# Kernel tuning notes

Measured on AMD Instinct MI355X. Metric: run time of the kernel, lower is better.

Reference implementation:

```python
import jax, jax.numpy as jnp
import numpy as np
from jax import lax


def setup_inputs() -> dict:
    key = jax.random.key(0)
    ks = jax.random.split(key, 5)
    B, Cin, H, W = 16, 64, 64, 64
    HID, K = 128, 3
    x = jax.random.normal(ks[0], (B, Cin, H, W), jnp.float32)
    w_is = jax.random.normal(ks[1], (4 * HID, Cin, 1, K), jnp.float32) * 0.05
    b_is = jax.random.normal(ks[2], (4 * HID,), jnp.float32) * 0.05
    w_ss = jax.random.normal(ks[3], (4 * HID, HID, 1, K), jnp.float32) * 0.05
    b_ss = jax.random.normal(ks[4], (4 * HID,), jnp.float32) * 0.05
    return {"x": x, "w_is": w_is, "b_is": b_is, "w_ss": w_ss, "b_ss": b_ss}


def reference(x, w_is, b_is, w_ss, b_ss):
    # Shapes: x [B,Cin,H,W]; w_is [4h,Cin,1,k]; w_ss [4h,h,1,k]
    hid = w_ss.shape[1]
    k = w_is.shape[-1]
    pad = k // 2

    # MaskedConv2d mask type 'B' on a (1,k) kernel: keep center and left taps,
    # zero everything strictly right of center.
    mask = (jnp.arange(k) <= pad).astype(x.dtype)  # [k]
    w_is_m = w_is * mask[None, None, None, :]

    # Input-to-state conv over the whole image at once: [B,4h,H,W]
    z_is = lax.conv_general_dilated(
        x, w_is_m, window_strides=(1, 1), padding=[(0, 0), (pad, pad)]
    ) + b_is[None, :, None, None]

    # State-to-state conv is a 1D conv along W: kernel [4h, h, k]
    w1 = w_ss[:, :, 0, :]

    def step(carry, z_row):
        h, c = carry  # each [B, hid, W]
        z = z_row + lax.conv_general_dilated(
            h, w1, window_strides=(1,), padding=[(pad, pad)],
            dimension_numbers=("NCH", "OIH", "NCH"),
        ) + b_ss[None, :, None]
        i_g = jax.nn.sigmoid(z[:, :hid])
        f_g = jax.nn.sigmoid(z[:, hid:2 * hid])
        o_g = jax.nn.sigmoid(z[:, 2 * hid:3 * hid])
        g = jnp.tanh(z[:, 3 * hid:])
        c = f_g * c + i_g * g
        h = o_g * jnp.tanh(c)
        return (h, c), h

    B, _, H, W = x.shape
    h0 = jnp.zeros((B, hid, W), x.dtype)
    c0 = jnp.zeros((B, hid, W), x.dtype)
    zs = jnp.transpose(z_is, (2, 0, 1, 3))  # [H, B, 4h, W]
    _, hs = lax.scan(step, (h0, c0), zs)    # hs: [H, B, hid, W]
    return jnp.transpose(hs, (1, 2, 0, 3))  # [B, hid, H, W]
```

## Files before the change

kernel.cpp:

```cpp
#include <hip/hip_runtime.h>
#include <hip/hip_bf16.h>

#define B_    16
#define CIN   64
#define Hn    64
#define Wn    64
#define HID   128
#define SXS2  72
#define SHS   136
#define NJC   8
#define NBLK  (B_ * NJC)

typedef __attribute__((ext_vector_type(8))) short bfrag_t;
typedef __attribute__((ext_vector_type(4))) float f4_t;

#define HBUF_SHORTS (B_ * Wn * HID)
#define HBUF_BYTES  (HBUF_SHORTS * 2)
#define FLG_STRIDE  256

static __device__ __forceinline__ short f2bf(float f) {
    union { __hip_bfloat16 h; short s; } u;
    u.h = __float2bfloat16(f);
    return u.s;
}
static __device__ __forceinline__ float sigm(float z)  { return 1.f / (1.f + __expf(-z)); }
static __device__ __forceinline__ float tanhf_(float z){ return 2.f / (1.f + __expf(-2.f * z)) - 1.f; }

#define BAR_LGKM() do { \
    asm volatile("s_waitcnt lgkmcnt(0)" ::: "memory"); \
    __builtin_amdgcn_s_barrier(); \
    __builtin_amdgcn_sched_barrier(0); \
} while (0)

extern "C" __global__ __launch_bounds__(256, 1)
void rowlstm_kernel(const float* __restrict__ x,
                    const float* __restrict__ w_is,
                    const float* __restrict__ b_is,
                    const float* __restrict__ w_ss,
                    const float* __restrict__ b_ss,
                    float* __restrict__ out,
                    unsigned char* __restrict__ ws)
{
    const int tid  = threadIdx.x;
    const int bid  = blockIdx.x;
    const int b    = bid & 15;
    const int jc   = bid >> 4;
    const int lane = tid & 63;
    const int wv   = tid >> 6;
    const int l15  = lane & 15;
    const int quad = lane >> 4;

    short*    hbuf0 = (short*)ws;
    unsigned* flags = (unsigned*)(ws + 2 * HBUF_BYTES + b * FLG_STRIDE);

    __shared__ alignas(16) short sH[66 * SHS];
    __shared__ alignas(16) short sX2[65 * SXS2];

    bfrag_t a_frag[4][16];
    #pragma unroll
    for (int mt = 0; mt < 4; ++mt) {
        const int co = mt * HID + jc * 16 + l15;
        #pragma unroll
        for (int kt = 0; kt < 16; ++kt) {
            const int kk0 = kt * 32 + quad * 8;
            const float* p;
            if      (kt < 2)  p = &w_is[(co * CIN + kk0)         * 3 + 0];
            else if (kt < 4)  p = &w_is[(co * CIN + (kk0 - 64))  * 3 + 1];
            else if (kt < 8)  p = &w_ss[(co * HID + (kk0 - 128)) * 3 + 0];
            else if (kt < 12) p = &w_ss[(co * HID + (kk0 - 256)) * 3 + 1];
            else              p = &w_ss[(co * HID + (kk0 - 384)) * 3 + 2];
            bfrag_t v;
            #pragma unroll
            for (int j = 0; j < 8; ++j) v[j] = f2bf(p[j * 3]);
            a_frag[mt][kt] = v;
        }
    }

    float bias[4][4];
    #pragma unroll
    for (int g = 0; g < 4; ++g) {
        #pragma unroll
        for (int r = 0; r < 4; ++r) {
            const int co = g * HID + jc * 16 + quad * 4 + r;
            bias[g][r] = b_is[co] + b_ss[co];
        }
    }

    {
        bfrag_t z8 = {0,0,0,0,0,0,0,0};
        if (tid < 8)  *(bfrag_t*)&sX2[tid * 8] = z8;
        if (tid < 16) {
            *(bfrag_t*)&sH[tid * 8] = z8;
            *(bfrag_t*)&sH[65 * SHS + tid * 8] = z8;
        }
    }

    float creg[4] = {0.f, 0.f, 0.f, 0.f};
    const int wp  = wv * 16 + l15;

    const int xw  = tid & 63;
    const int xc2 = tid >> 6;
    float xr[16];
    #pragma unroll
    for (int e = 0; e < 16; ++e)
        xr[e] = x[((b * CIN + xc2 * 16 + e) * Hn + 0) * Wn + xw];

    {
        bfrag_t v0, v1;
        #pragma unroll
        for (int e = 0; e < 8; ++e) { v0[e] = f2bf(xr[e]); v1[e] = f2bf(xr[e + 8]); }
        *(bfrag_t*)&sX2[(xw + 1) * SXS2 + xc2 * 16]     = v0;
        *(bfrag_t*)&sX2[(xw + 1) * SXS2 + xc2 * 16 + 8] = v1;
        #pragma unroll
        for (int e = 0; e < 16; ++e)
            xr[e] = x[((b * CIN + xc2 * 16 + e) * Hn + 1) * Wn + xw];
    }

    const int cig = tid & 15;
    const int w0  = tid >> 4;

    __syncthreads();

    for (int h = 0; h < Hn; ++h) {
        const short* rd_hb = hbuf0 + ((h & 1) ^ 1) * HBUF_SHORTS + b * Wn * HID;
        short*       wr_hb = hbuf0 + (h & 1) * HBUF_SHORTS + b * Wn * HID;

        union { bfrag_t f; unsigned long long q[2]; } hu0, hu1, hu2, hu3;
        if (h > 0) {
            const unsigned tgt = (unsigned)h;
            for (;;) {
                unsigned f = __hip_atomic_load(&flags[lane & 31],
                                               __ATOMIC_RELAXED, __HIP_MEMORY_SCOPE_AGENT);
                if (__all((int)(f >= tgt))) break;
                __builtin_amdgcn_s_sleep(1);
            }
            asm volatile("" ::: "memory");

            const unsigned long long* s0 = (const unsigned long long*)(rd_hb + (w0     ) * HID + cig * 8);
            const unsigned long long* s1 = (const unsigned long long*)(rd_hb + (w0 + 16) * HID + cig * 8);
            const unsigned long long* s2 = (const unsigned long long*)(rd_hb + (w0 + 32) * HID + cig * 8);
            const unsigned long long* s3 = (const unsigned long long*)(rd_hb + (w0 + 48) * HID + cig * 8);
            hu0.q[0] = __hip_atomic_load(s0,     __ATOMIC_RELAXED, __HIP_MEMORY_SCOPE_AGENT);
            hu0.q[1] = __hip_atomic_load(s0 + 1, __ATOMIC_RELAXED, __HIP_MEMORY_SCOPE_AGENT);
            hu1.q[0] = __hip_atomic_load(s1,     __ATOMIC_RELAXED, __HIP_MEMORY_SCOPE_AGENT);
            hu1.q[1] = __hip_atomic_load(s1 + 1, __ATOMIC_RELAXED, __HIP_MEMORY_SCOPE_AGENT);
            hu2.q[0] = __hip_atomic_load(s2,     __ATOMIC_RELAXED, __HIP_MEMORY_SCOPE_AGENT);
            hu2.q[1] = __hip_atomic_load(s2 + 1, __ATOMIC_RELAXED, __HIP_MEMORY_SCOPE_AGENT);
            hu3.q[0] = __hip_atomic_load(s3,     __ATOMIC_RELAXED, __HIP_MEMORY_SCOPE_AGENT);
            hu3.q[1] = __hip_atomic_load(s3 + 1, __ATOMIC_RELAXED, __HIP_MEMORY_SCOPE_AGENT);
        } else {
            hu0.q[0] = hu0.q[1] = 0ull; hu1.q[0] = hu1.q[1] = 0ull;
            hu2.q[0] = hu2.q[1] = 0ull; hu3.q[0] = hu3.q[1] = 0ull;
        }

        f4_t acc0 = {0.f,0.f,0.f,0.f}, acc1 = {0.f,0.f,0.f,0.f};
        f4_t acc2 = {0.f,0.f,0.f,0.f}, acc3 = {0.f,0.f,0.f,0.f};
        #pragma unroll
        for (int kt = 0; kt < 4; ++kt) {
            const short* src = &sX2[(wp + (kt >> 1)) * SXS2 + (kt & 1) * 32 + quad * 8];
            bfrag_t bf = *(const bfrag_t*)src;
            acc0 = __builtin_amdgcn_mfma_f32_16x16x32_bf16(a_frag[0][kt], bf, acc0, 0, 0, 0);
            acc1 = __builtin_amdgcn_mfma_f32_16x16x32_bf16(a_frag[1][kt], bf, acc1, 0, 0, 0);
            acc2 = __builtin_amdgcn_mfma_f32_16x16x32_bf16(a_frag[2][kt], bf, acc2, 0, 0, 0);
            acc3 = __builtin_amdgcn_mfma_f32_16x16x32_bf16(a_frag[3][kt], bf, acc3, 0, 0, 0);
        }

        *(bfrag_t*)&sH[(w0 +  1) * SHS + cig * 8] = hu0.f;
        *(bfrag_t*)&sH[(w0 + 17) * SHS + cig * 8] = hu1.f;
        *(bfrag_t*)&sH[(w0 + 33) * SHS + cig * 8] = hu2.f;
        *(bfrag_t*)&sH[(w0 + 49) * SHS + cig * 8] = hu3.f;
        BAR_LGKM();

        #pragma unroll
        for (int kt = 4; kt < 16; ++kt) {
            const short* src = &sH[(wp + ((kt - 4) >> 2)) * SHS + ((kt - 4) & 3) * 32 + quad * 8];
            bfrag_t bf = *(const bfrag_t*)src;
            acc0 = __builtin_amdgcn_mfma_f32_16x16x32_bf16(a_frag[0][kt], bf, acc0, 0, 0, 0);
            acc1 = __builtin_amdgcn_mfma_f32_16x16x32_bf16(a_frag[1][kt], bf, acc1, 0, 0, 0);
            acc2 = __builtin_amdgcn_mfma_f32_16x16x32_bf16(a_frag[2][kt], bf, acc2, 0, 0, 0);
            acc3 = __builtin_amdgcn_mfma_f32_16x16x32_bf16(a_frag[3][kt], bf, acc3, 0, 0, 0);
        }

        float hv[4];
        #pragma unroll
        for (int r = 0; r < 4; ++r) {
            float ig = sigm (acc0[r] + bias[0][r]);
            float fg = sigm (acc1[r] + bias[1][r]);
            float og = sigm (acc2[r] + bias[2][r]);
            float gg = tanhf_(acc3[r] + bias[3][r]);
            float c  = fg * creg[r] + ig * gg;
            creg[r]  = c;
            hv[r]    = og * tanhf_(c);
        }

        if (h + 1 < Hn) {
            unsigned p0 = (unsigned)(unsigned short)f2bf(hv[0]) |
                          ((unsigned)(unsigned short)f2bf(hv[1]) << 16);
            unsigned p1 = (unsigned)(unsigned short)f2bf(hv[2]) |
                          ((unsigned)(unsigned short)f2bf(hv[3]) << 16);
            unsigned long long pk = (unsigned long long)p0 | ((unsigned long long)p1 << 32);
            __hip_atomic_store((unsigned long long*)(wr_hb + wp * HID + jc * 16 + quad * 4),
                               pk, __ATOMIC_RELAXED, __HIP_MEMORY_SCOPE_AGENT);
            asm volatile("s_waitcnt vmcnt(0)" ::: "memory");
            if (lane == 0)
                __hip_atomic_store(&flags[jc * 4 + wv], (unsigned)(h + 1),
                                   __ATOMIC_RELAXED, __HIP_MEMORY_SCOPE_AGENT);
        }

        __syncthreads();

        if (h + 1 < Hn) {
            bfrag_t v0, v1;
            #pragma unroll
            for (int e = 0; e < 8; ++e) { v0[e] = f2bf(xr[e]); v1[e] = f2bf(xr[e + 8]); }
            *(bfrag_t*)&sX2[(xw + 1) * SXS2 + xc2 * 16]     = v0;
            *(bfrag_t*)&sX2[(xw + 1) * SXS2 + xc2 * 16 + 8] = v1;
        }

        #pragma unroll
        for (int r = 0; r < 4; ++r)
            out[((b * HID + jc * 16 + quad * 4 + r) * Hn + h) * Wn + wp] = hv[r];

        if (h + 2 < Hn) {
            #pragma unroll
            for (int e = 0; e < 16; ++e)
                xr[e] = x[((b * CIN + xc2 * 16 + e) * Hn + (h + 2)) * Wn + xw];
        }

        if (h + 1 < Hn)
            BAR_LGKM();
    }
}

extern "C" void kernel_launch(void* const* d_in, const int* in_sizes, int n_in,
                              void* d_out, int out_size, void* d_ws, size_t ws_size,
                              hipStream_t stream) {
    const float* x    = (const float*)d_in[0];
    const float* w_is = (const float*)d_in[1];
    const float* b_is = (const float*)d_in[2];
    const float* w_ss = (const float*)d_in[3];
    const float* b_ss = (const float*)d_in[4];
    float* out = (float*)d_out;
    unsigned char* ws = (unsigned char*)d_ws;

    hipMemsetAsync(ws + 2 * HBUF_BYTES, 0, B_ * FLG_STRIDE, stream);

    rowlstm_kernel<<<dim3(NBLK), dim3(256), 0, stream>>>(x, w_is, b_is, w_ss, b_ss, out, ws);
}
```

Baseline: 314.2 us.

## Co-locate each batch's blocks on one XCD and exchange state via local L2

Launches 256 blocks and has each one read its XCD id from a hardware register, then claim a role so that the 8 blocks sharing a batch element land on the same XCD when possible. Excess blocks exit. When a batch's group is all on one XCD, hidden state and flags go through an extra buffer using plain stores and sc0 loads that stay in the local L2 rather than agent-scope coherent accesses. This aims to cut the latency of the per-row inter-block handoff. It keeps a coherent fallback path with a poll timeout and dual-writes every row, which adds store traffic. It also relies on unverified assumptions about L2 coherence and the hwreg layout.

```diff
diff --git a/kernel.cpp b/kernel.cpp
--- a/kernel.cpp
+++ b/kernel.cpp
@@ -9,14 +9,18 @@
 #define SXS2  72
 #define SHS   136
 #define NJC   8
-#define NBLK  (B_ * NJC)
+#define NGRID 256
+#define POLL_TO 256
 
 typedef __attribute__((ext_vector_type(8))) short bfrag_t;
 typedef __attribute__((ext_vector_type(4))) float f4_t;
 
 #define HBUF_SHORTS (B_ * Wn * HID)
 #define HBUF_BYTES  (HBUF_SHORTS * 2)
-#define FLG_STRIDE  256
+#define DATA_A_OFF  0
+#define DATA_B_OFF  (2 * HBUF_BYTES)
+#define FLG_OFF     (4 * HBUF_BYTES)
+#define CLAIM_OFF   (FLG_OFF + B_ * 256)
 
 static __device__ __forceinline__ short f2bf(float f) {
     union { __hip_bfloat16 h; short s; } u;
@@ -42,16 +46,58 @@
                     unsigned char* __restrict__ ws)
 {
     const int tid  = threadIdx.x;
-    const int bid  = blockIdx.x;
-    const int b    = bid & 15;
-    const int jc   = bid >> 4;
     const int lane = tid & 63;
     const int wv   = tid >> 6;
     const int l15  = lane & 15;
     const int quad = lane >> 4;
 
-    short*    hbuf0 = (short*)ws;
-    unsigned* flags = (unsigned*)(ws + 2 * HBUF_BYTES + b * FLG_STRIDE);
+    __shared__ int sB, sJ, sM;
+    if (tid == 0) {
+        unsigned* cl = (unsigned*)(ws + CLAIM_OFF);
+        unsigned xcd;
+        asm volatile("s_getreg_b32 %0, hwreg(20, 0, 32)" : "=s"(xcd));
+        xcd &= 7u;
+        unsigned slot = __hip_atomic_fetch_add(&cl[xcd], 1u, __ATOMIC_RELAXED, __HIP_MEMORY_SCOPE_AGENT);
+        int role = (slot < 16u) ? (int)(xcd * 16u + slot) : -1;
+        __hip_atomic_fetch_add(&cl[8], 1u, __ATOMIC_RELEASE, __HIP_MEMORY_SCOPE_AGENT);
+        if (role < 0) {
+            while (__hip_atomic_load(&cl[8], __ATOMIC_ACQUIRE, __HIP_MEMORY_SCOPE_AGENT) < (unsigned)NGRID)
+                __builtin_amdgcn_s_sleep(8);
+            unsigned ovr = __hip_atomic_fetch_add(&cl[9], 1u, __ATOMIC_RELAXED, __HIP_MEMORY_SCOPE_AGENT);
+            unsigned base = 0;
+            for (int k = 0; k < 8 && role < 0; ++k) {
+                unsigned c = __hip_atomic_load(&cl[k], __ATOMIC_RELAXED, __HIP_MEMORY_SCOPE_AGENT);
+                if (c > 16u) c = 16u;
+                unsigned miss = 16u - c;
+                if (ovr < base + miss) role = (int)(k * 16u + c + (ovr - base));
+                base += miss;
+            }
+        }
+        int bb = -1, jj = 0, mm = 0;
+        if (role >= 0) {
+            bb = (role >> 4) * 2 + ((role >> 3) & 1);
+            jj = role & 7;
+            __hip_atomic_store(&cl[32 + bb * 8 + jj], xcd + 1u, __ATOMIC_RELAXED, __HIP_MEMORY_SCOPE_AGENT);
+            __hip_atomic_fetch_add(&cl[16 + bb], 1u, __ATOMIC_RELEASE, __HIP_MEMORY_SCOPE_AGENT);
+            while (__hip_atomic_load(&cl[16 + bb], __ATOMIC_ACQUIRE, __HIP_MEMORY_SCOPE_AGENT) < 8u)
+                __builtin_amdgcn_s_sleep(8);
+            mm = 1;
+            for (int j = 0; j < 8; ++j)
+                if (__hip_atomic_load(&cl[32 + bb * 8 + j], __ATOMIC_RELAXED, __HIP_MEMORY_SCOPE_AGENT) != xcd + 1u)
+                    mm = 0;
+        }
+        sB = bb; sJ = jj; sM = mm;
+    }
+    __syncthreads();
+    const int  b   = sB;
+    const int  jc  = sJ;
+    const bool l2m = (sM != 0);
+    if (b < 0) return;
+
+    short*    hbufA = (short*)(ws + DATA_A_OFF);
+    short*    hbufB = (short*)(ws + DATA_B_OFF);
+    unsigned* flgA  = (unsigned*)(ws + FLG_OFF + b * 256);
+    unsigned* flgB  = flgA + 32;
 
     __shared__ alignas(16) short sH[66 * SHS];
     __shared__ alignas(16) short sX2[65 * SXS2];
@@ -104,7 +150,6 @@
     #pragma unroll
     for (int e = 0; e < 16; ++e)
         xr[e] = x[((b * CIN + xc2 * 16 + e) * Hn + 0) * Wn + xw];
-
     {
         bfrag_t v0, v1;
         #pragma unroll
@@ -118,39 +163,78 @@
 
     const int cig = tid & 15;
     const int w0  = tid >> 4;
+    const unsigned long long spinA = (unsigned long long)(flgA + (lane & 31));
+    int fastok = l2m ? 1 : 0, failn = 0;
 
     __syncthreads();
 
     for (int h = 0; h < Hn; ++h) {
-        const short* rd_hb = hbuf0 + ((h & 1) ^ 1) * HBUF_SHORTS + b * Wn * HID;
-        short*       wr_hb = hbuf0 + (h & 1) * HBUF_SHORTS + b * Wn * HID;
-
-        union { bfrag_t f; unsigned long long q[2]; } hu0, hu1, hu2, hu3;
+        const int    par = (h & 1) ^ 1;
+        const short* rdA = hbufA + par * HBUF_SHORTS + b * Wn * HID;
+        const short* rdB = hbufB + par * HBUF_SHORTS + b * Wn * HID;
+        short*       wrA = hbufA + (h & 1) * HBUF_SHORTS + b * Wn * HID;
+        short*       wrB = hbufB + (h & 1) * HBUF_SHORTS + b * Wn * HID;
+
+        bfrag_t f0, f1, f2, f3;
         if (h > 0) {
             const unsigned tgt = (unsigned)h;
-            for (;;) {
-                unsigned f = __hip_atomic_load(&flags[lane & 31],
-                                               __ATOMIC_RELAXED, __HIP_MEMORY_SCOPE_AGENT);
-                if (__all((int)(f >= tgt))) break;
-                __builtin_amdgcn_s_sleep(1);
+            bool fast = false;
+            if (fastok) {
+                int iters = 0;
+                for (;;) {
+                    unsigned f;
+                    asm volatile("global_load_dword %0, %1, off sc0\n\t"
+                                 "s_waitcnt vmcnt(0)"
+                                 : "=v"(f) : "v"(spinA) : "memory");
+                    if (__all((int)(f >= tgt))) { fast = true; break; }
+                    if (++iters > POLL_TO) break;
+                    __builtin_amdgcn_s_sleep(1);
+                }
+                if (!fast && ++failn >= 2) fastok = 0;
+            }
+            if (!fast) {
+                for (;;) {
+                    unsigned f = __hip_atomic_load(&flgB[lane & 31],
+                                                   __ATOMIC_RELAXED, __HIP_MEMORY_SCOPE_AGENT);
+                    if (__all((int)(f >= tgt))) break;
+                    __builtin_amdgcn_s_sleep(1);
+                }
             }
             asm volatile("" ::: "memory");
 
-            const unsigned long long* s0 = (const unsigned long long*)(rd_hb + (w0     ) * HID + cig * 8);
-            const unsigned long long* s1 = (const unsigned long long*)(rd_hb + (w0 + 16) * HID + cig * 8);
-            const unsigned long long* s2 = (const unsigned long long*)(rd_hb + (w0 + 32) * HID + cig * 8);
-            const unsigned long long* s3 = (const unsigned long long*)(rd_hb + (w0 + 48) * HID + cig * 8);
-            hu0.q[0] = __hip_atomic_load(s0,     __ATOMIC_RELAXED, __HIP_MEMORY_SCOPE_AGENT);
-            hu0.q[1] = __hip_atomic_load(s0 + 1, __ATOMIC_RELAXED, __HIP_MEMORY_SCOPE_AGENT);
-            hu1.q[0] = __hip_atomic_load(s1,     __ATOMIC_RELAXED, __HIP_MEMORY_SCOPE_AGENT);
-            hu1.q[1] = __hip_atomic_load(s1 + 1, __ATOMIC_RELAXED, __HIP_MEMORY_SCOPE_AGENT);
-            hu2.q[0] = __hip_atomic_load(s2,     __ATOMIC_RELAXED, __HIP_MEMORY_SCOPE_AGENT);
-            hu2.q[1] = __hip_atomic_load(s2 + 1, __ATOMIC_RELAXED, __HIP_MEMORY_SCOPE_AGENT);
-            hu3.q[0] = __hip_atomic_load(s3,     __ATOMIC_RELAXED, __HIP_MEMORY_SCOPE_AGENT);
-            hu3.q[1] = __hip_atomic_load(s3 + 1, __ATOMIC_RELAXED, __HIP_MEMORY_SCOPE_AGENT);
+            if (fast) {
+                const unsigned long long a0 = (unsigned long long)(rdA + (w0     ) * HID + cig * 8);
+                const unsigned long long a1 = (unsigned long long)(rdA + (w0 + 16) * HID + cig * 8);
+                const unsigned long long a2 = (unsigned long long)(rdA + (w0 + 32) * HID + cig * 8);
+                const unsigned long long a3 = (unsigned long long)(rdA + (w0 + 48) * HID + cig * 8);
+                asm volatile("global_load_dwordx4 %0, %4, off sc0\n\t"
+                             "global_load_dwordx4 %1, %5, off sc0\n\t"
+                             "global_load_dwordx4 %2, %6, off sc0\n\t"
+                             "global_load_dwordx4 %3, %7, off sc0\n\t"
+                             "s_waitcnt vmcnt(0)"
+                             : "=&v"(f0), "=&v"(f1), "=&v"(f2), "=&v"(f3)
+                             : "v"(a0), "v"(a1), "v"(a2), "v"(a3)
+                             : "memory");
+                __builtin_amdgcn_sched_barrier(0);
+            } else {
+                union { bfrag_t f; unsigned long long q[2]; } u0, u1, u2, u3;
+                const unsigned long long* s0 = (const unsigned long long*)(rdB + (w0     ) * HID + cig * 8);
+                const unsigned long long* s1 = (const unsigned long long*)(rdB + (w0 + 16) * HID + cig * 8);
+                const unsigned long long* s2 = (const unsigned long long*)(rdB + (w0 + 32) * HID + cig * 8);
+                const unsigned long long* s3 = (const unsigned long long*)(rdB + (w0 + 48) * HID + cig * 8);
+                u0.q[0] = __hip_atomic_load(s0,     __ATOMIC_RELAXED, __HIP_MEMORY_SCOPE_AGENT);
+                u0.q[1] = __hip_atomic_load(s0 + 1, __ATOMIC_RELAXED, __HIP_MEMORY_SCOPE_AGENT);
+                u1.q[0] = __hip_atomic_load(s1,     __ATOMIC_RELAXED, __HIP_MEMORY_SCOPE_AGENT);
+                u1.q[1] = __hip_atomic_load(s1 + 1, __ATOMIC_RELAXED, __HIP_MEMORY_SCOPE_AGENT);
+                u2.q[0] = __hip_atomic_load(s2,     __ATOMIC_RELAXED, __HIP_MEMORY_SCOPE_AGENT);
+                u2.q[1] = __hip_atomic_load(s2 + 1, __ATOMIC_RELAXED, __HIP_MEMORY_SCOPE_AGENT);
+                u3.q[0] = __hip_atomic_load(s3,     __ATOMIC_RELAXED, __HIP_MEMORY_SCOPE_AGENT);
+                u3.q[1] = __hip_atomic_load(s3 + 1, __ATOMIC_RELAXED, __HIP_MEMORY_SCOPE_AGENT);
+                f0 = u0.f; f1 = u1.f; f2 = u2.f; f3 = u3.f;
+            }
         } else {
-            hu0.q[0] = hu0.q[1] = 0ull; hu1.q[0] = hu1.q[1] = 0ull;
-            hu2.q[0] = hu2.q[1] = 0ull; hu3.q[0] = hu3.q[1] = 0ull;
+            bfrag_t z8 = {0,0,0,0,0,0,0,0};
+            f0 = z8; f1 = z8; f2 = z8; f3 = z8;
         }
 
         f4_t acc0 = {0.f,0.f,0.f,0.f}, acc1 = {0.f,0.f,0.f,0.f};
@@ -165,10 +249,10 @@
             acc3 = __builtin_amdgcn_mfma_f32_16x16x32_bf16(a_frag[3][kt], bf, acc3, 0, 0, 0);
         }
 
-        *(bfrag_t*)&sH[(w0 +  1) * SHS + cig * 8] = hu0.f;
-        *(bfrag_t*)&sH[(w0 + 17) * SHS + cig * 8] = hu1.f;
-        *(bfrag_t*)&sH[(w0 + 33) * SHS + cig * 8] = hu2.f;
-        *(bfrag_t*)&sH[(w0 + 49) * SHS + cig * 8] = hu3.f;
+        *(bfrag_t*)&sH[(w0 +  1) * SHS + cig * 8] = f0;
+        *(bfrag_t*)&sH[(w0 + 17) * SHS + cig * 8] = f1;
+        *(bfrag_t*)&sH[(w0 + 33) * SHS + cig * 8] = f2;
+        *(bfrag_t*)&sH[(w0 + 49) * SHS + cig * 8] = f3;
         BAR_LGKM();
 
         #pragma unroll
@@ -199,11 +283,22 @@
             unsigned p1 = (unsigned)(unsigned short)f2bf(hv[2]) |
                           ((unsigned)(unsigned short)f2bf(hv[3]) << 16);
             unsigned long long pk = (unsigned long long)p0 | ((unsigned long long)p1 << 32);
-            __hip_atomic_store((unsigned long long*)(wr_hb + wp * HID + jc * 16 + quad * 4),
-                               pk, __ATOMIC_RELAXED, __HIP_MEMORY_SCOPE_AGENT);
+            const int doff = wp * HID + jc * 16 + quad * 4;
+            const unsigned nxt = (unsigned)(h + 1);
+            if (l2m) {
+                const unsigned long long aA = (unsigned long long)(wrA + doff);
+                asm volatile("global_store_dwordx2 %0, %1, off" :: "v"(aA), "v"(pk) : "memory");
+                asm volatile("s_waitcnt vmcnt(0)" ::: "memory");
+                if (lane == 0) {
+                    const unsigned long long fA = (unsigned long long)(flgA + jc * 4 + wv);
+                    asm volatile("global_store_dword %0, %1, off" :: "v"(fA), "v"(nxt) : "memory");
+                }
+            }
+            __hip_atomic_store((unsigned long long*)(wrB + doff), pk,
+                               __ATOMIC_RELAXED, __HIP_MEMORY_SCOPE_AGENT);
             asm volatile("s_waitcnt vmcnt(0)" ::: "memory");
             if (lane == 0)
-                __hip_atomic_store(&flags[jc * 4 + wv], (unsigned)(h + 1),
+                __hip_atomic_store(&flgB[jc * 4 + wv], nxt,
                                    __ATOMIC_RELAXED, __HIP_MEMORY_SCOPE_AGENT);
         }
 
@@ -243,7 +338,7 @@
     float* out = (float*)d_out;
     unsigned char* ws = (unsigned char*)d_ws;
 
-    hipMemsetAsync(ws + 2 * HBUF_BYTES, 0, B_ * FLG_STRIDE, stream);
-
-    rowlstm_kernel<<<dim3(NBLK), dim3(256), 0, stream>>>(x, w_is, b_is, w_ss, b_ss, out, ws);
+    hipMemsetAsync(ws + FLG_OFF, 0, B_ * 256 + 1024, stream);
+
+    rowlstm_kernel<<<dim3(NGRID), dim3(256), 0, stream>>>(x, w_is, b_is, w_ss, b_ss, out, ws);
 }
```

After: 391.1 us. +24.5%, slower.
